# Kernel tuning notes

Hardware: AMD Instinct MI355X
Metric: run time of the kernel (lower is better)

The kernel has to match this reference:

```python
import jax, jax.numpy as jnp
import numpy as np

N = 10000      # nodes
E = 160000     # edges
D_IN = 512
D_H = 512
P_DROP = 0.2


def _glorot(key, shape):
    lim = float(np.sqrt(6.0 / (shape[0] + shape[1])))
    return jax.random.uniform(key, shape, jnp.float32, -lim, lim)


def setup_inputs() -> dict:
    key = jax.random.key(0)
    ks = jax.random.split(key, 8)
    h = jax.random.normal(ks[0], (N, D_IN), jnp.float32)
    src = jax.random.randint(ks[1], (E,), 0, N)
    dst = jax.random.randint(ks[2], (E,), 0, N)
    edge_weight = jax.random.uniform(ks[3], (E,), jnp.float32)
    W0 = _glorot(ks[4], (D_IN, D_H))
    W1 = _glorot(ks[5], (D_H, D_H))
    W2 = _glorot(ks[6], (D_H, D_H))
    b0 = jnp.zeros((D_H,), jnp.float32)
    b1 = jnp.zeros((D_H,), jnp.float32)
    b2 = jnp.zeros((D_H,), jnp.float32)
    return dict(h=h, src=src, dst=dst, edge_weight=edge_weight,
                W0=W0, b0=b0, W1=W1, b1=b1, W2=W2, b2=b2)


def _dropout(x, key):
    keep = jax.random.bernoulli(key, 1.0 - P_DROP, x.shape)
    return jnp.where(keep, x / (1.0 - P_DROP), 0.0)


def _graph_conv(x, src, dst, ew, W, b, act):
    # DGL GraphConv, norm='both', weight=True, bias=True, with edge_weight.
    ones = jnp.ones((src.shape[0],), x.dtype)
    deg_out = jnp.maximum(jax.ops.segment_sum(ones, src, num_segments=N), 1.0)
    deg_in = jnp.maximum(jax.ops.segment_sum(ones, dst, num_segments=N), 1.0)
    x = x * (deg_out ** -0.5)[:, None]          # src norm
    msg = x[src] * ew[:, None]                  # [E, D] gather + edge weight
    agg = jax.ops.segment_sum(msg, dst, num_segments=N)  # scatter-add
    out = (agg @ W) * (deg_in ** -0.5)[:, None] + b
    return act(out) if act is not None else out


def reference(h, src, dst, edge_weight, W0, b0, W1, b1, W2, b2):
    dk = jax.random.split(jax.random.key(42), 3)
    x = _dropout(h, dk[0])
    x = _graph_conv(x, src, dst, edge_weight, W0, b0, jax.nn.elu)
    x = _dropout(x, dk[1])
    x = _graph_conv(x, src, dst, edge_weight, W1, b1, jax.nn.elu)
    x = _dropout(x, dk[2])
    x = _graph_conv(x, src, dst, edge_weight, W2, b2, None)
    return x
```

## Files before the change

### kernel.cpp

```cpp
#include <hip/hip_runtime.h>
#include <stdint.h>

#define N_NODES 10000
#define N_EDGES 160000
#define D 512
#define TOT (N_NODES * D)
#define MASK_DW (TOT / 32)
#define FM 64
#define LDAF 520

typedef _Float16 h8 __attribute__((ext_vector_type(8)));
typedef float f4 __attribute__((ext_vector_type(4)));

__host__ __device__ inline uint32_t rotl32(uint32_t v, int r) {
    return (v << r) | (v >> (32 - r));
}

__host__ __device__ inline void tf2x32(uint32_t k0, uint32_t k1,
                                       uint32_t& x0, uint32_t& x1) {
    uint32_t k2 = k0 ^ k1 ^ 0x1BD11BDAu;
    x0 += k0; x1 += k1;
    x0 += x1; x1 = rotl32(x1, 13); x1 ^= x0;
    x0 += x1; x1 = rotl32(x1, 15); x1 ^= x0;
    x0 += x1; x1 = rotl32(x1, 26); x1 ^= x0;
    x0 += x1; x1 = rotl32(x1,  6); x1 ^= x0;
    x0 += k1; x1 += k2 + 1u;
    x0 += x1; x1 = rotl32(x1, 17); x1 ^= x0;
    x0 += x1; x1 = rotl32(x1, 29); x1 ^= x0;
    x0 += x1; x1 = rotl32(x1, 16); x1 ^= x0;
    x0 += x1; x1 = rotl32(x1, 24); x1 ^= x0;
    x0 += k2; x1 += k0 + 2u;
    x0 += x1; x1 = rotl32(x1, 13); x1 ^= x0;
    x0 += x1; x1 = rotl32(x1, 15); x1 ^= x0;
    x0 += x1; x1 = rotl32(x1, 26); x1 ^= x0;
    x0 += x1; x1 = rotl32(x1,  6); x1 ^= x0;
    x0 += k0; x1 += k1 + 3u;
    x0 += x1; x1 = rotl32(x1, 17); x1 ^= x0;
    x0 += x1; x1 = rotl32(x1, 29); x1 ^= x0;
    x0 += x1; x1 = rotl32(x1, 16); x1 ^= x0;
    x0 += x1; x1 = rotl32(x1, 24); x1 ^= x0;
    x0 += k1; x1 += k2 + 4u;
    x0 += x1; x1 = rotl32(x1, 13); x1 ^= x0;
    x0 += x1; x1 = rotl32(x1, 15); x1 ^= x0;
    x0 += x1; x1 = rotl32(x1, 26); x1 ^= x0;
    x0 += x1; x1 = rotl32(x1,  6); x1 ^= x0;
    x0 += k2; x1 += k0 + 5u;
}

__device__ __forceinline__ float dropout_gate(uint32_t k0, uint32_t k1, uint32_t j) {
    uint32_t c0 = 0u, c1 = j;
    tf2x32(k0, k1, c0, c1);
    uint32_t bits = c0 ^ c1;
    float u = __uint_as_float((bits >> 9) | 0x3f800000u) - 1.0f;
    return (u < 0.8f) ? 1.0f : 0.0f;
}

__global__ __launch_bounds__(256)
void mask_kernel(uint32_t* __restrict__ mask, uint32_t k0a, uint32_t k1a,
                 uint32_t k0b, uint32_t k1b) {
    int t = blockIdx.x * 256 + threadIdx.x;
    int layer = (t >= MASK_DW) ? 1 : 0;
    uint32_t k0 = layer ? k0b : k0a;
    uint32_t k1 = layer ? k1b : k1a;
    uint32_t base = (uint32_t)(layer ? t - MASK_DW : t) * 32u;
    uint32_t m = 0;
#pragma unroll
    for (int i = 0; i < 32; ++i) {
        uint32_t c0 = 0u, c1 = base + (uint32_t)i;
        tf2x32(k0, k1, c0, c1);
        uint32_t bits = c0 ^ c1;
        float u = __uint_as_float((bits >> 9) | 0x3f800000u) - 1.0f;
        m |= (u < 0.8f ? 1u : 0u) << i;
    }
    mask[t] = m;
}

__global__ void hist_kernel(const int* __restrict__ src, const int* __restrict__ dst,
                            int* __restrict__ deg_out, int* __restrict__ deg_in) {
    int e = blockIdx.x * 256 + threadIdx.x;
    if (e >= N_EDGES) return;
    atomicAdd(&deg_out[src[e]], 1);
    atomicAdd(&deg_in[dst[e]], 1);
}

__global__ __launch_bounds__(1024)
void scan_kernel(const int* __restrict__ deg_in, const int* __restrict__ deg_out,
                 int* __restrict__ row_ptr,
                 float* __restrict__ rn_in, float* __restrict__ rn_out) {
    __shared__ int wsum[16];
    __shared__ int base_s;
    int tid = threadIdx.x;
    int lane = tid & 63, wv = tid >> 6;
    if (tid == 0) base_s = 0;
    __syncthreads();
    for (int start = 0; start < N_NODES; start += 1024) {
        int i = start + tid;
        int v = (i < N_NODES) ? deg_in[i] : 0;
        int s = v;
#pragma unroll
        for (int off = 1; off < 64; off <<= 1) {
            int t = __shfl_up(s, off, 64);
            if (lane >= off) s += t;
        }
        if (lane == 63) wsum[wv] = s;
        __syncthreads();
        if (wv == 0 && lane < 16) {
            int ws = wsum[lane];
#pragma unroll
            for (int off = 1; off < 16; off <<= 1) {
                int t = __shfl_up(ws, off, 64);
                if (lane >= off) ws += t;
            }
            wsum[lane] = ws;
        }
        __syncthreads();
        if (i < N_NODES) {
            int prefix = base_s + ((wv > 0) ? wsum[wv - 1] : 0) + (s - v);
            row_ptr[i] = prefix;
            rn_in[i]  = 1.0f / sqrtf(fmaxf((float)v, 1.0f));
            rn_out[i] = 1.0f / sqrtf(fmaxf((float)deg_out[i], 1.0f));
        }
        __syncthreads();
        if (tid == 0) base_s += wsum[15];
        __syncthreads();
    }
    if (tid == 0) row_ptr[N_NODES] = base_s;
}

__global__ void fill_kernel(const int* __restrict__ src, const int* __restrict__ dst,
                            const float* __restrict__ ew, const int* __restrict__ row_ptr,
                            int* __restrict__ cursor, int2* __restrict__ csr) {
    int e = blockIdx.x * 256 + threadIdx.x;
    if (e >= N_EDGES) return;
    int v = dst[e];
    int pos = atomicAdd(&cursor[v], 1);
    int idx = row_ptr[v] + pos;
    csr[idx] = make_int2(src[e], __float_as_int(ew[e]));
}

__global__ __launch_bounds__(256)
void wconvert_kernel(const float* __restrict__ W0, const float* __restrict__ W1,
                     const float* __restrict__ W2, _Float16* __restrict__ Wt) {
    __shared__ float tile[64][65];
    const float* W = (blockIdx.z == 0) ? W0 : (blockIdx.z == 1) ? W1 : W2;
    _Float16* T = Wt + (size_t)blockIdx.z * 512 * 512;
    int r0 = blockIdx.y * 64, c0 = blockIdx.x * 64;
    int t = threadIdx.x;
    int c = t & 63, rq = t >> 6;
#pragma unroll
    for (int i = 0; i < 16; ++i) {
        int r = rq + i * 4;
        tile[r][c] = W[(size_t)(r0 + r) * 512 + c0 + c];
    }
    __syncthreads();
    int k = t & 63, nq = t >> 6;
#pragma unroll
    for (int i = 0; i < 16; ++i) {
        int n = nq + i * 4;
        T[(size_t)(c0 + n) * 512 + r0 + k] = (_Float16)tile[k][n];
    }
}

__global__ __launch_bounds__(256)
void dropout_kernel(const float* __restrict__ x, _Float16* __restrict__ y,
                    const float* __restrict__ rn_out, uint32_t k0, uint32_t k1) {
    int t = blockIdx.x * 256 + threadIdx.x;
    int j = t * 4;
    if (j >= TOT) return;
    float4 xv = *(const float4*)&x[j];
    float w = rn_out[j >> 9];
    _Float16 r[4];
    uint32_t jj = (uint32_t)j;
#pragma unroll
    for (int i = 0; i < 4; ++i) {
        float g = dropout_gate(k0, k1, jj + (uint32_t)i);
        float xi = (&xv.x)[i];
        r[i] = (_Float16)(g * (xi / 0.8f) * w);
    }
    *(ushort4*)&y[j] = *(ushort4*)r;
}

__global__ __launch_bounds__(1024, 4)
void layer_kernel(const _Float16* __restrict__ yin, const int* __restrict__ row_ptr,
                  const int2* __restrict__ csr, const _Float16* __restrict__ Wt,
                  const float* __restrict__ bias, const float* __restrict__ rn_in,
                  const float* __restrict__ rn_out, const uint32_t* __restrict__ mask,
                  _Float16* __restrict__ yout, float* __restrict__ fout, int mode) {
    __shared__ _Float16 As[FM * LDAF];
    int tid = threadIdx.x;
    int wv = tid >> 6, lane = tid & 63;
    int row0 = blockIdx.x * FM;

#pragma unroll 1
    for (int nn = 0; nn < 4; ++nn) {
        int ln = wv * 4 + nn;
        int node = row0 + ln;
        float acc[8] = {0, 0, 0, 0, 0, 0, 0, 0};
        if (node < N_NODES) {
            int beg = row_ptr[node], end = row_ptr[node + 1];
            int k = beg;
            for (; k + 7 < end; k += 8) {
                h8 a[8];
                float w[8];
#pragma unroll
                for (int q = 0; q < 8; ++q) {
                    int2 e = csr[k + q];
                    a[q] = *(const h8*)&yin[(size_t)e.x * 512 + lane * 8];
                    w[q] = __int_as_float(e.y);
                }
#pragma unroll
                for (int q = 0; q < 8; ++q)
#pragma unroll
                    for (int i = 0; i < 8; ++i) acc[i] += w[q] * (float)a[q][i];
            }
            for (; k + 3 < end; k += 4) {
                h8 a[4];
                float w[4];
#pragma unroll
                for (int q = 0; q < 4; ++q) {
                    int2 e = csr[k + q];
                    a[q] = *(const h8*)&yin[(size_t)e.x * 512 + lane * 8];
                    w[q] = __int_as_float(e.y);
                }
#pragma unroll
                for (int q = 0; q < 4; ++q)
#pragma unroll
                    for (int i = 0; i < 8; ++i) acc[i] += w[q] * (float)a[q][i];
            }
            for (; k < end; ++k) {
                int2 e0 = csr[k];
                float w0 = __int_as_float(e0.y);
                h8 a = *(const h8*)&yin[(size_t)e0.x * 512 + lane * 8];
#pragma unroll
                for (int i = 0; i < 8; ++i) acc[i] += w0 * (float)a[i];
            }
        }
        _Float16 r[8];
#pragma unroll
        for (int i = 0; i < 8; ++i) r[i] = (_Float16)acc[i];
        *(h8*)&As[ln * LDAF + lane * 8] = *(h8*)r;
    }
    __syncthreads();

    f4 acc[4][2];
#pragma unroll
    for (int i = 0; i < 4; ++i)
#pragma unroll
        for (int j = 0; j < 2; ++j) acc[i][j] = (f4){0.f, 0.f, 0.f, 0.f};

    int kf = (lane >> 4) * 8;
    const _Float16* fa = &As[(lane & 15) * LDAF + kf];
    int col0 = wv * 32;
    const _Float16* gB0 = Wt + (size_t)(col0 + (lane & 15)) * 512 + kf;
    const _Float16* gB1 = gB0 + (size_t)16 * 512;

#pragma unroll 4
    for (int kk = 0; kk < 512; kk += 32) {
        h8 af[4], bf0, bf1;
        bf0 = *(const h8*)(gB0 + kk);
        bf1 = *(const h8*)(gB1 + kk);
#pragma unroll
        for (int mt = 0; mt < 4; ++mt)
            af[mt] = *(const h8*)(fa + mt * 16 * LDAF + kk);
#pragma unroll
        for (int mt = 0; mt < 4; ++mt) {
            acc[mt][0] = __builtin_amdgcn_mfma_f32_16x16x32_f16(af[mt], bf0,
                                                                acc[mt][0], 0, 0, 0);
            acc[mt][1] = __builtin_amdgcn_mfma_f32_16x16x32_f16(af[mt], bf1,
                                                                acc[mt][1], 0, 0, 0);
        }
    }

#pragma unroll
    for (int mt = 0; mt < 4; ++mt) {
#pragma unroll
        for (int nt = 0; nt < 2; ++nt) {
            int gr0 = row0 + mt * 16 + (lane >> 4) * 4;
            int gc = col0 + nt * 16 + (lane & 15);
            float bcol = bias[gc];
#pragma unroll
            for (int i = 0; i < 4; ++i) {
                int gr = gr0 + i;
                if (gr >= N_NODES) continue;
                float v = acc[mt][nt][i] * rn_in[gr] + bcol;
                if (mode == 0) {
                    v = (v > 0.f) ? v : expm1f(v);
                    uint32_t m = mask[gr * 16 + (gc >> 5)];
                    float keep = (float)((m >> (gc & 31)) & 1u);
                    v = keep * (v / 0.8f) * rn_out[gr];
                    yout[(size_t)gr * 512 + gc] = (_Float16)v;
                } else {
                    fout[(size_t)gr * 512 + gc] = v;
                }
            }
        }
    }
}

extern "C" void kernel_launch(void* const* d_in, const int* in_sizes, int n_in,
                              void* d_out, int out_size, void* d_ws, size_t ws_size,
                              hipStream_t stream) {
    const float* h   = (const float*)d_in[0];
    const int*   src = (const int*)d_in[1];
    const int*   dst = (const int*)d_in[2];
    const float* ew  = (const float*)d_in[3];
    const float* W0  = (const float*)d_in[4];
    const float* b0  = (const float*)d_in[5];
    const float* W1  = (const float*)d_in[6];
    const float* b1  = (const float*)d_in[7];
    const float* W2  = (const float*)d_in[8];
    const float* b2  = (const float*)d_in[9];
    const float* bl[3] = {b0, b1, b2};
    float* out = (float*)d_out;

    char* ws = (char*)d_ws;
    _Float16* yA   = (_Float16*)ws; ws += (size_t)TOT * 2;
    _Float16* yB   = (_Float16*)ws; ws += (size_t)TOT * 2;
    _Float16* Wt   = (_Float16*)ws; ws += (size_t)3 * 512 * 512 * 2;
    uint32_t* mask = (uint32_t*)ws; ws += (size_t)2 * MASK_DW * 4;
    int* degi_in  = (int*)ws;  ws += N_NODES * 4;
    int* degi_out = (int*)ws;  ws += N_NODES * 4;
    int* cursor   = (int*)ws;  ws += N_NODES * 4;
    int* row_ptr  = (int*)ws;  ws += (N_NODES + 1) * 4;
    ws = (char*)(((uintptr_t)ws + 15) & ~(uintptr_t)15);
    int2* csr     = (int2*)ws; ws += (size_t)N_EDGES * 8;
    float* rn_in  = (float*)ws; ws += N_NODES * 4;
    float* rn_out = (float*)ws; ws += N_NODES * 4;

    hipMemsetAsync(degi_in, 0, 3 * N_NODES * 4, stream);

    uint32_t dk[3][2];
    for (int i = 0; i < 3; ++i) {
        uint32_t c0 = 0u, c1 = (uint32_t)i;
        tf2x32(0u, 42u, c0, c1);
        dk[i][0] = c0; dk[i][1] = c1;
    }

    mask_kernel<<<(2 * MASK_DW) / 256, 256, 0, stream>>>(mask, dk[1][0], dk[1][1],
                                                         dk[2][0], dk[2][1]);
    hist_kernel<<<(N_EDGES + 255) / 256, 256, 0, stream>>>(src, dst, degi_out, degi_in);
    scan_kernel<<<1, 1024, 0, stream>>>(degi_in, degi_out, row_ptr, rn_in, rn_out);
    fill_kernel<<<(N_EDGES + 255) / 256, 256, 0, stream>>>(src, dst, ew, row_ptr,
                                                           cursor, csr);
    wconvert_kernel<<<dim3(8, 8, 3), 256, 0, stream>>>(W0, W1, W2, Wt);

    dropout_kernel<<<(TOT / 4 + 255) / 256, 256, 0, stream>>>(h, yA, rn_out,
                                                              dk[0][0], dk[0][1]);
    const int NBLK = (N_NODES + FM - 1) / FM;
    layer_kernel<<<NBLK, 1024, 0, stream>>>(yA, row_ptr, csr, Wt, bl[0],
                                            rn_in, rn_out, mask, yB, out, 0);
    layer_kernel<<<NBLK, 1024, 0, stream>>>(yB, row_ptr, csr, Wt + (size_t)512 * 512,
                                            bl[1], rn_in, rn_out, mask + MASK_DW,
                                            yA, out, 0);
    layer_kernel<<<NBLK, 1024, 0, stream>>>(yA, row_ptr, csr, Wt + (size_t)2 * 512 * 512,
                                            bl[2], rn_in, rn_out, nullptr,
                                            nullptr, out, 1);
}
```

Before: 324.8 us.

## Merge setup kernels, single-pass scan, and shrink layer tiles to 16 rows

Combines histogram, mask generation and weight conversion into one launch, and CSR fill with input dropout into another, cutting launch count. The scan kernel now does a single pass with each thread handling 10 nodes instead of looping over chunks. The layer kernel moves to 16-row tiles with 256 threads, so each wave computes 128 output columns and 625 blocks run instead of 157. Bounds checks are dropped because 10000 divides evenly by 16. This trades more weight reloads per block for better occupancy and load balance on the gather.

```diff
diff --git a/kernel.cpp b/kernel.cpp
--- a/kernel.cpp
+++ b/kernel.cpp
@@ -6,8 +6,14 @@
 #define D 512
 #define TOT (N_NODES * D)
 #define MASK_DW (TOT / 32)
-#define FM 64
+#define FM 16
 #define LDAF 520
+
+#define HIST_B 625
+#define MASK_B 1250
+#define WCV_B  192
+#define FILL_B 625
+#define DROP_B 5000
 
 typedef _Float16 h8 __attribute__((ext_vector_type(8)));
 typedef float f4 __attribute__((ext_vector_type(4)));
@@ -56,31 +62,58 @@
 }
 
 __global__ __launch_bounds__(256)
-void mask_kernel(uint32_t* __restrict__ mask, uint32_t k0a, uint32_t k1a,
-                 uint32_t k0b, uint32_t k1b) {
-    int t = blockIdx.x * 256 + threadIdx.x;
-    int layer = (t >= MASK_DW) ? 1 : 0;
-    uint32_t k0 = layer ? k0b : k0a;
-    uint32_t k1 = layer ? k1b : k1a;
-    uint32_t base = (uint32_t)(layer ? t - MASK_DW : t) * 32u;
-    uint32_t m = 0;
-#pragma unroll
-    for (int i = 0; i < 32; ++i) {
-        uint32_t c0 = 0u, c1 = base + (uint32_t)i;
-        tf2x32(k0, k1, c0, c1);
-        uint32_t bits = c0 ^ c1;
-        float u = __uint_as_float((bits >> 9) | 0x3f800000u) - 1.0f;
-        m |= (u < 0.8f ? 1u : 0u) << i;
-    }
-    mask[t] = m;
-}
-
-__global__ void hist_kernel(const int* __restrict__ src, const int* __restrict__ dst,
-                            int* __restrict__ deg_out, int* __restrict__ deg_in) {
-    int e = blockIdx.x * 256 + threadIdx.x;
-    if (e >= N_EDGES) return;
-    atomicAdd(&deg_out[src[e]], 1);
-    atomicAdd(&deg_in[dst[e]], 1);
+void setup1_kernel(const int* __restrict__ src, const int* __restrict__ dst,
+                   int* __restrict__ deg_out, int* __restrict__ deg_in,
+                   uint32_t* __restrict__ mask,
+                   uint32_t k0a, uint32_t k1a, uint32_t k0b, uint32_t k1b,
+                   const float* __restrict__ W0, const float* __restrict__ W1,
+                   const float* __restrict__ W2, _Float16* __restrict__ Wt) {
+    __shared__ float tile[64][65];
+    int b = blockIdx.x;
+    int tid = threadIdx.x;
+    if (b < HIST_B) {
+        int e = b * 256 + tid;
+        if (e < N_EDGES) {
+            atomicAdd(&deg_out[src[e]], 1);
+            atomicAdd(&deg_in[dst[e]], 1);
+        }
+    } else if (b < HIST_B + MASK_B) {
+        int t = (b - HIST_B) * 256 + tid;
+        int layer = (t >= MASK_DW) ? 1 : 0;
+        uint32_t k0 = layer ? k0b : k0a;
+        uint32_t k1 = layer ? k1b : k1a;
+        uint32_t base = (uint32_t)(layer ? t - MASK_DW : t) * 32u;
+        uint32_t m = 0;
+#pragma unroll
+        for (int i = 0; i < 32; ++i) {
+            uint32_t c0 = 0u, c1 = base + (uint32_t)i;
+            tf2x32(k0, k1, c0, c1);
+            uint32_t bits = c0 ^ c1;
+            float u = __uint_as_float((bits >> 9) | 0x3f800000u) - 1.0f;
+            m |= (u < 0.8f ? 1u : 0u) << i;
+        }
+        mask[t] = m;
+    } else {
+        int q = b - (HIST_B + MASK_B);
+        int bz = q >> 6, r = q & 63;
+        int by = r >> 3, bx = r & 7;
+        const float* W = (bz == 0) ? W0 : (bz == 1) ? W1 : W2;
+        _Float16* T = Wt + (size_t)bz * 512 * 512;
+        int r0 = by * 64, c0 = bx * 64;
+        int c = tid & 63, rq = tid >> 6;
+#pragma unroll
+        for (int i = 0; i < 16; ++i) {
+            int rr = rq + i * 4;
+            tile[rr][c] = W[(size_t)(r0 + rr) * 512 + c0 + c];
+        }
+        __syncthreads();
+        int k = tid & 63, nq = tid >> 6;
+#pragma unroll
+        for (int i = 0; i < 16; ++i) {
+            int n = nq + i * 4;
+            T[(size_t)(c0 + n) * 512 + r0 + k] = (_Float16)tile[k][n];
+        }
+    }
 }
 
 __global__ __launch_bounds__(1024)
@@ -88,99 +121,88 @@
                  int* __restrict__ row_ptr,
                  float* __restrict__ rn_in, float* __restrict__ rn_out) {
     __shared__ int wsum[16];
-    __shared__ int base_s;
     int tid = threadIdx.x;
     int lane = tid & 63, wv = tid >> 6;
-    if (tid == 0) base_s = 0;
+    int base = tid * 10;
+    bool act = base < N_NODES;
+    int d[10];
+#pragma unroll
+    for (int j = 0; j < 10; ++j) d[j] = 0;
+    if (act) {
+#pragma unroll
+        for (int j = 0; j < 10; ++j) d[j] = deg_in[base + j];
+    }
+    int tot = 0;
+#pragma unroll
+    for (int j = 0; j < 10; ++j) tot += d[j];
+    int s = tot;
+#pragma unroll
+    for (int off = 1; off < 64; off <<= 1) {
+        int u = __shfl_up(s, off, 64);
+        if (lane >= off) s += u;
+    }
+    if (lane == 63) wsum[wv] = s;
     __syncthreads();
-    for (int start = 0; start < N_NODES; start += 1024) {
-        int i = start + tid;
-        int v = (i < N_NODES) ? deg_in[i] : 0;
-        int s = v;
-#pragma unroll
-        for (int off = 1; off < 64; off <<= 1) {
-            int t = __shfl_up(s, off, 64);
-            if (lane >= off) s += t;
-        }
-        if (lane == 63) wsum[wv] = s;
-        __syncthreads();
-        if (wv == 0 && lane < 16) {
-            int ws = wsum[lane];
-#pragma unroll
-            for (int off = 1; off < 16; off <<= 1) {
-                int t = __shfl_up(ws, off, 64);
-                if (lane >= off) ws += t;
-            }
-            wsum[lane] = ws;
-        }
-        __syncthreads();
-        if (i < N_NODES) {
-            int prefix = base_s + ((wv > 0) ? wsum[wv - 1] : 0) + (s - v);
-            row_ptr[i] = prefix;
+    if (wv == 0 && lane < 16) {
+        int ws = wsum[lane];
+#pragma unroll
+        for (int off = 1; off < 16; off <<= 1) {
+            int u = __shfl_up(ws, off, 64);
+            if (lane >= off) ws += u;
+        }
+        wsum[lane] = ws;
+    }
+    __syncthreads();
+    if (act) {
+        int run = ((wv > 0) ? wsum[wv - 1] : 0) + (s - tot);
+#pragma unroll
+        for (int j = 0; j < 10; ++j) {
+            int i = base + j;
+            row_ptr[i] = run;
+            int v = d[j];
             rn_in[i]  = 1.0f / sqrtf(fmaxf((float)v, 1.0f));
             rn_out[i] = 1.0f / sqrtf(fmaxf((float)deg_out[i], 1.0f));
-        }
-        __syncthreads();
-        if (tid == 0) base_s += wsum[15];
-        __syncthreads();
-    }
-    if (tid == 0) row_ptr[N_NODES] = base_s;
-}
-
-__global__ void fill_kernel(const int* __restrict__ src, const int* __restrict__ dst,
-                            const float* __restrict__ ew, const int* __restrict__ row_ptr,
-                            int* __restrict__ cursor, int2* __restrict__ csr) {
-    int e = blockIdx.x * 256 + threadIdx.x;
-    if (e >= N_EDGES) return;
-    int v = dst[e];
-    int pos = atomicAdd(&cursor[v], 1);
-    int idx = row_ptr[v] + pos;
-    csr[idx] = make_int2(src[e], __float_as_int(ew[e]));
+            run += v;
+        }
+    }
+    if (tid == 0) row_ptr[N_NODES] = wsum[15];
 }
 
 __global__ __launch_bounds__(256)
-void wconvert_kernel(const float* __restrict__ W0, const float* __restrict__ W1,
-                     const float* __restrict__ W2, _Float16* __restrict__ Wt) {
-    __shared__ float tile[64][65];
-    const float* W = (blockIdx.z == 0) ? W0 : (blockIdx.z == 1) ? W1 : W2;
-    _Float16* T = Wt + (size_t)blockIdx.z * 512 * 512;
-    int r0 = blockIdx.y * 64, c0 = blockIdx.x * 64;
-    int t = threadIdx.x;
-    int c = t & 63, rq = t >> 6;
-#pragma unroll
-    for (int i = 0; i < 16; ++i) {
-        int r = rq + i * 4;
-        tile[r][c] = W[(size_t)(r0 + r) * 512 + c0 + c];
-    }
-    __syncthreads();
-    int k = t & 63, nq = t >> 6;
-#pragma unroll
-    for (int i = 0; i < 16; ++i) {
-        int n = nq + i * 4;
-        T[(size_t)(c0 + n) * 512 + r0 + k] = (_Float16)tile[k][n];
+void setup2_kernel(const int* __restrict__ src, const int* __restrict__ dst,
+                   const float* __restrict__ ew, const int* __restrict__ row_ptr,
+                   int* __restrict__ cursor, int2* __restrict__ csr,
+                   const float* __restrict__ x, _Float16* __restrict__ y,
+                   const float* __restrict__ rn_out, uint32_t k0, uint32_t k1) {
+    int b = blockIdx.x;
+    int tid = threadIdx.x;
+    if (b < FILL_B) {
+        int e = b * 256 + tid;
+        if (e < N_EDGES) {
+            int v = dst[e];
+            int pos = atomicAdd(&cursor[v], 1);
+            csr[row_ptr[v] + pos] = make_int2(src[e], __float_as_int(ew[e]));
+        }
+    } else {
+        int t = (b - FILL_B) * 256 + tid;
+        int j = t * 4;
+        if (j < TOT) {
+            float4 xv = *(const float4*)&x[j];
+            float w = rn_out[j >> 9];
+            _Float16 r[4];
+            uint32_t jj = (uint32_t)j;
+#pragma unroll
+            for (int i = 0; i < 4; ++i) {
+                float g = dropout_gate(k0, k1, jj + (uint32_t)i);
+                float xi = (&xv.x)[i];
+                r[i] = (_Float16)(g * (xi / 0.8f) * w);
+            }
+            *(ushort4*)&y[j] = *(ushort4*)r;
+        }
     }
 }
 
 __global__ __launch_bounds__(256)
-void dropout_kernel(const float* __restrict__ x, _Float16* __restrict__ y,
-                    const float* __restrict__ rn_out, uint32_t k0, uint32_t k1) {
-    int t = blockIdx.x * 256 + threadIdx.x;
-    int j = t * 4;
-    if (j >= TOT) return;
-    float4 xv = *(const float4*)&x[j];
-    float w = rn_out[j >> 9];
-    _Float16 r[4];
-    uint32_t jj = (uint32_t)j;
-#pragma unroll
-    for (int i = 0; i < 4; ++i) {
-        float g = dropout_gate(k0, k1, jj + (uint32_t)i);
-        float xi = (&xv.x)[i];
-        r[i] = (_Float16)(g * (xi / 0.8f) * w);
-    }
-    *(ushort4*)&y[j] = *(ushort4*)r;
-}
-
-__global__ __launch_bounds__(1024, 4)
 void layer_kernel(const _Float16* __restrict__ yin, const int* __restrict__ row_ptr,
                   const int2* __restrict__ csr, const _Float16* __restrict__ Wt,
                   const float* __restrict__ bias, const float* __restrict__ rn_in,
@@ -196,44 +218,42 @@
         int ln = wv * 4 + nn;
         int node = row0 + ln;
         float acc[8] = {0, 0, 0, 0, 0, 0, 0, 0};
-        if (node < N_NODES) {
-            int beg = row_ptr[node], end = row_ptr[node + 1];
-            int k = beg;
-            for (; k + 7 < end; k += 8) {
-                h8 a[8];
-                float w[8];
-#pragma unroll
-                for (int q = 0; q < 8; ++q) {
-                    int2 e = csr[k + q];
-                    a[q] = *(const h8*)&yin[(size_t)e.x * 512 + lane * 8];
-                    w[q] = __int_as_float(e.y);
-                }
-#pragma unroll
-                for (int q = 0; q < 8; ++q)
-#pragma unroll
-                    for (int i = 0; i < 8; ++i) acc[i] += w[q] * (float)a[q][i];
+        int beg = row_ptr[node], end = row_ptr[node + 1];
+        int k = beg;
+        for (; k + 7 < end; k += 8) {
+            h8 a[8];
+            float w[8];
+#pragma unroll
+            for (int q = 0; q < 8; ++q) {
+                int2 e = csr[k + q];
+                a[q] = *(const h8*)&yin[(size_t)e.x * 512 + lane * 8];
+                w[q] = __int_as_float(e.y);
             }
-            for (; k + 3 < end; k += 4) {
-                h8 a[4];
-                float w[4];
-#pragma unroll
-                for (int q = 0; q < 4; ++q) {
-                    int2 e = csr[k + q];
-                    a[q] = *(const h8*)&yin[(size_t)e.x * 512 + lane * 8];
-                    w[q] = __int_as_float(e.y);
-                }
-#pragma unroll
-                for (int q = 0; q < 4; ++q)
-#pragma unroll
-                    for (int i = 0; i < 8; ++i) acc[i] += w[q] * (float)a[q][i];
+#pragma unroll
+            for (int q = 0; q < 8; ++q)
+#pragma unroll
+                for (int i = 0; i < 8; ++i) acc[i] += w[q] * (float)a[q][i];
+        }
+        for (; k + 3 < end; k += 4) {
+            h8 a[4];
+            float w[4];
+#pragma unroll
+            for (int q = 0; q < 4; ++q) {
+                int2 e = csr[k + q];
+                a[q] = *(const h8*)&yin[(size_t)e.x * 512 + lane * 8];
+                w[q] = __int_as_float(e.y);
             }
-            for (; k < end; ++k) {
-                int2 e0 = csr[k];
-                float w0 = __int_as_float(e0.y);
-                h8 a = *(const h8*)&yin[(size_t)e0.x * 512 + lane * 8];
-#pragma unroll
-                for (int i = 0; i < 8; ++i) acc[i] += w0 * (float)a[i];
-            }
+#pragma unroll
+            for (int q = 0; q < 4; ++q)
+#pragma unroll
+                for (int i = 0; i < 8; ++i) acc[i] += w[q] * (float)a[q][i];
+        }
+        for (; k < end; ++k) {
+            int2 e0 = csr[k];
+            float w0 = __int_as_float(e0.y);
+            h8 a = *(const h8*)&yin[(size_t)e0.x * 512 + lane * 8];
+#pragma unroll
+            for (int i = 0; i < 8; ++i) acc[i] += w0 * (float)a[i];
         }
         _Float16 r[8];
 #pragma unroll
@@ -242,56 +262,45 @@
     }
     __syncthreads();
 
-    f4 acc[4][2];
-#pragma unroll
-    for (int i = 0; i < 4; ++i)
-#pragma unroll
-        for (int j = 0; j < 2; ++j) acc[i][j] = (f4){0.f, 0.f, 0.f, 0.f};
+    f4 acc[8];
+#pragma unroll
+    for (int i = 0; i < 8; ++i) acc[i] = (f4){0.f, 0.f, 0.f, 0.f};
 
     int kf = (lane >> 4) * 8;
     const _Float16* fa = &As[(lane & 15) * LDAF + kf];
-    int col0 = wv * 32;
-    const _Float16* gB0 = Wt + (size_t)(col0 + (lane & 15)) * 512 + kf;
-    const _Float16* gB1 = gB0 + (size_t)16 * 512;
-
-#pragma unroll 4
+    int col0 = wv * 128;
+    const _Float16* gB = Wt + (size_t)(col0 + (lane & 15)) * 512 + kf;
+
+#pragma unroll 2
     for (int kk = 0; kk < 512; kk += 32) {
-        h8 af[4], bf0, bf1;
-        bf0 = *(const h8*)(gB0 + kk);
-        bf1 = *(const h8*)(gB1 + kk);
-#pragma unroll
-        for (int mt = 0; mt < 4; ++mt)
-            af[mt] = *(const h8*)(fa + mt * 16 * LDAF + kk);
-#pragma unroll
-        for (int mt = 0; mt < 4; ++mt) {
-            acc[mt][0] = __builtin_amdgcn_mfma_f32_16x16x32_f16(af[mt], bf0,
-                                                                acc[mt][0], 0, 0, 0);
-            acc[mt][1] = __builtin_amdgcn_mfma_f32_16x16x32_f16(af[mt], bf1,
-                                                                acc[mt][1], 0, 0, 0);
-        }
-    }
-
-#pragma unroll
-    for (int mt = 0; mt < 4; ++mt) {
-#pragma unroll
-        for (int nt = 0; nt < 2; ++nt) {
-            int gr0 = row0 + mt * 16 + (lane >> 4) * 4;
-            int gc = col0 + nt * 16 + (lane & 15);
-            float bcol = bias[gc];
-#pragma unroll
-            for (int i = 0; i < 4; ++i) {
-                int gr = gr0 + i;
-                if (gr >= N_NODES) continue;
-                float v = acc[mt][nt][i] * rn_in[gr] + bcol;
-                if (mode == 0) {
-                    v = (v > 0.f) ? v : expm1f(v);
-                    uint32_t m = mask[gr * 16 + (gc >> 5)];
-                    float keep = (float)((m >> (gc & 31)) & 1u);
-                    v = keep * (v / 0.8f) * rn_out[gr];
-                    yout[(size_t)gr * 512 + gc] = (_Float16)v;
-                } else {
-                    fout[(size_t)gr * 512 + gc] = v;
-                }
+        h8 af = *(const h8*)(fa + kk);
+        h8 bf[8];
+#pragma unroll
+        for (int nt = 0; nt < 8; ++nt)
+            bf[nt] = *(const h8*)(gB + (size_t)nt * 16 * 512 + kk);
+#pragma unroll
+        for (int nt = 0; nt < 8; ++nt)
+            acc[nt] = __builtin_amdgcn_mfma_f32_16x16x32_f16(af, bf[nt],
+                                                             acc[nt], 0, 0, 0);
+    }
+
+    int gr0 = row0 + (lane >> 4) * 4;
+#pragma unroll
+    for (int nt = 0; nt < 8; ++nt) {
+        int gc = col0 + nt * 16 + (lane & 15);
+        float bcol = bias[gc];
+#pragma unroll
+        for (int i = 0; i < 4; ++i) {
+            int gr = gr0 + i;
+            float v = acc[nt][i] * rn_in[gr] + bcol;
+            if (mode == 0) {
+                v = (v > 0.f) ? v : expm1f(v);
+                uint32_t m = mask[gr * 16 + (gc >> 5)];
+                float keep = (float)((m >> (gc & 31)) & 1u);
+                v = keep * (v / 0.8f) * rn_out[gr];
+                yout[(size_t)gr * 512 + gc] = (_Float16)v;
+            } else {
+                fout[(size_t)gr * 512 + gc] = v;
             }
         }
     }
@@ -336,23 +345,20 @@
         dk[i][0] = c0; dk[i][1] = c1;
     }
 
-    mask_kernel<<<(2 * MASK_DW) / 256, 256, 0, stream>>>(mask, dk[1][0], dk[1][1],
-                                                         dk[2][0], dk[2][1]);
-    hist_kernel<<<(N_EDGES + 255) / 256, 256, 0, stream>>>(src, dst, degi_out, degi_in);
+    setup1_kernel<<<HIST_B + MASK_B + WCV_B, 256, 0, stream>>>(
+        src, dst, degi_out, degi_in, mask,
+        dk[1][0], dk[1][1], dk[2][0], dk[2][1], W0, W1, W2, Wt);
     scan_kernel<<<1, 1024, 0, stream>>>(degi_in, degi_out, row_ptr, rn_in, rn_out);
-    fill_kernel<<<(N_EDGES + 255) / 256, 256, 0, stream>>>(src, dst, ew, row_ptr,
-                                                           cursor, csr);
-    wconvert_kernel<<<dim3(8, 8, 3), 256, 0, stream>>>(W0, W1, W2, Wt);
-
-    dropout_kernel<<<(TOT / 4 + 255) / 256, 256, 0, stream>>>(h, yA, rn_out,
-                                                              dk[0][0], dk[0][1]);
-    const int NBLK = (N_NODES + FM - 1) / FM;
-    layer_kernel<<<NBLK, 1024, 0, stream>>>(yA, row_ptr, csr, Wt, bl[0],
-                                            rn_in, rn_out, mask, yB, out, 0);
-    layer_kernel<<<NBLK, 1024, 0, stream>>>(yB, row_ptr, csr, Wt + (size_t)512 * 512,
-                                            bl[1], rn_in, rn_out, mask + MASK_DW,
-                                            yA, out, 0);
-    layer_kernel<<<NBLK, 1024, 0, stream>>>(yA, row_ptr, csr, Wt + (size_t)2 * 512 * 512,
-                                            bl[2], rn_in, rn_out, nullptr,
-                                            nullptr, out, 1);
-}
+    setup2_kernel<<<FILL_B + DROP_B, 256, 0, stream>>>(
+        src, dst, ew, row_ptr, cursor, csr, h, yA, rn_out, dk[0][0], dk[0][1]);
+
+    const int NBLK = N_NODES / FM;
+    layer_kernel<<<NBLK, 256, 0, stream>>>(yA, row_ptr, csr, Wt, bl[0],
+                                           rn_in, rn_out, mask, yB, out, 0);
+    layer_kernel<<<NBLK, 256, 0, stream>>>(yB, row_ptr, csr, Wt + (size_t)512 * 512,
+                                           bl[1], rn_in, rn_out, mask + MASK_DW,
+                                           yA, out, 0);
+    layer_kernel<<<NBLK, 256, 0, stream>>>(yA, row_ptr, csr, Wt + (size_t)2 * 512 * 512,
+                                           bl[2], rn_in, rn_out, nullptr,
+                                           nullptr, out, 1);
+}
```

Result: slower. 349.7 us (+7.7%).
